# Kernel tuning notes

Hardware: AMD Instinct MI355X
Metric: run time of the kernel (lower is better)

## Reference

```python
import jax, jax.numpy as jnp
import numpy as np

B, IN_DIM, EXP_DIM, E = 16384, 256, 128, 8  # batch, input_dim, expert_dim, expert_num


def setup_inputs() -> dict:
    key = jax.random.key(0)
    ks = jax.random.split(key, 12)
    s_in = 1.0 / np.sqrt(IN_DIM)
    return {
        "x_a": jax.random.normal(ks[0], (B, IN_DIM), jnp.float32),
        "x_b": jax.random.normal(ks[1], (B, IN_DIM), jnp.float32),
        "x_share": jax.random.normal(ks[2], (B, IN_DIM), jnp.float32),
        # expert banks: [E, IN_DIM, EXP_DIM] weights, [E, EXP_DIM] bias
        "Wa": jax.random.uniform(ks[3], (E, IN_DIM, EXP_DIM), jnp.float32, -s_in, s_in),
        "ba": jax.random.uniform(ks[4], (E, EXP_DIM), jnp.float32, -s_in, s_in),
        "Wb": jax.random.uniform(ks[5], (E, IN_DIM, EXP_DIM), jnp.float32, -s_in, s_in),
        "bb": jax.random.uniform(ks[6], (E, EXP_DIM), jnp.float32, -s_in, s_in),
        "Ws": jax.random.uniform(ks[7], (E, IN_DIM, EXP_DIM), jnp.float32, -s_in, s_in),
        "bs": jax.random.uniform(ks[8], (E, EXP_DIM), jnp.float32, -s_in, s_in),
        # gate projections (bias=False): num single-output linears == one [num, IN_DIM] matrix
        "Ga": jax.random.uniform(ks[9], (2 * E, IN_DIM), jnp.float32, -s_in, s_in),
        "Gb": jax.random.uniform(ks[10], (2 * E, IN_DIM), jnp.float32, -s_in, s_in),
        "Gs": jax.random.uniform(ks[11], (3 * E, IN_DIM), jnp.float32, -s_in, s_in),
    }


def _experts(x, W, b):
    # batched dense stack: [B,IN] x [E,IN,D] -> [B,E,D]
    return jnp.einsum("bi,eid->bed", x, W) + b[None, :, :]


def _gate(x, G, experts):
    # logits [B, num]; softmax over experts; weighted sum over expert axis
    w = jax.nn.softmax(x @ G.T, axis=1)
    return jnp.einsum("be,bed->bd", w, experts)


def reference(x_a, x_b, x_share, Wa, ba, Wb, bb, Ws, bs, Ga, Gb, Gs):
    ea = _experts(x_a, Wa, ba)          # [B,E,D]
    eb = _experts(x_b, Wb, bb)          # [B,E,D]
    es = _experts(x_share, Ws, bs)      # [B,E,D]
    out_a = _gate(x_a, Ga, jnp.concatenate([ea, es], axis=1))
    out_b = _gate(x_b, Gb, jnp.concatenate([eb, es], axis=1))
    out_s = _gate(x_share, Gs, jnp.concatenate([ea, eb, es], axis=1))
    return (out_a, out_b, out_s)
```

## Files before the change

kernel.cpp:

```cpp
#include <hip/hip_runtime.h>
#include <stdint.h>

#define BATCH 16384
#define INDIM 256
#define DDIM  128
#define NEXP  8
#define ROWS  64
#define THREADS 512
#define NSTEP 192
#define RINGD 8

typedef __bf16 bfv8  __attribute__((ext_vector_type(8)));
typedef float  f32x4 __attribute__((ext_vector_type(4)));

typedef __attribute__((address_space(1))) const void gas_void;
typedef __attribute__((address_space(3))) void las_void;

__global__ void prep_kernel(const float* __restrict__ Wa, const float* __restrict__ Wb,
                            const float* __restrict__ Ws, const float* __restrict__ Ga,
                            const float* __restrict__ Gb, const float* __restrict__ Gs,
                            __bf16* __restrict__ wp, __bf16* __restrict__ gp) {
    int t = blockIdx.x * 256 + threadIdx.x;
    const int NW = 3 * 8 * 8 * 8 * 64;
    if (t < NW) {
        int lane = t & 63, nt = (t >> 6) & 7, kt = (t >> 9) & 7, e = (t >> 12) & 7, st = t >> 15;
        const float* W = (st == 0) ? Wa : (st == 1) ? Wb : Ws;
        int d  = nt * 16 + (lane & 15);
        int i0 = kt * 32 + (lane >> 4) * 8;
        __bf16* o = wp + (size_t)t * 8;
#pragma unroll
        for (int j = 0; j < 8; j++)
            o[j] = (__bf16)W[(size_t)(e * 256 + i0 + j) * 128 + d];
    } else if (t < NW + 2048) {
        int t2 = t - NW;
        int lane = t2 & 63, nt = (t2 >> 6) & 3, kt = t2 >> 8;
        int g  = nt * 16 + (lane & 15);
        int k0 = kt * 32 + (lane >> 4) * 8;
        __bf16* o = gp + (size_t)t2 * 8;
#pragma unroll
        for (int j = 0; j < 8; j++) {
            int k = k0 + j;
            float v = 0.f;
            if (g < 16)      v = Ga[g * 256 + k];
            else if (g < 32) v = Gb[(g - 16) * 256 + k];
            else if (g < 56) v = Gs[(g - 32) * 256 + k];
            o[j] = (__bf16)v;
        }
    }
}

__device__ __forceinline__ void load_afr(const float* __restrict__ x, int rb,
                                         int l16, int quad, bfv8 afr[2][8]) {
#pragma unroll
    for (int mt = 0; mt < 2; mt++) {
        const float* xr = x + (size_t)(rb + mt * 16 + l16) * INDIM;
#pragma unroll
        for (int kt = 0; kt < 8; kt++) {
            const f32x4* p = (const f32x4*)(xr + kt * 32 + quad * 8);
            f32x4 lo = __builtin_nontemporal_load(p);
            f32x4 hi = __builtin_nontemporal_load(p + 1);
            bfv8 a;
            a[0] = (__bf16)lo[0]; a[1] = (__bf16)lo[1]; a[2] = (__bf16)lo[2]; a[3] = (__bf16)lo[3];
            a[4] = (__bf16)hi[0]; a[5] = (__bf16)hi[1]; a[6] = (__bf16)hi[2]; a[7] = (__bf16)hi[3];
            afr[mt][kt] = a;
        }
    }
}

__device__ __forceinline__ void stage_step(const __bf16* __restrict__ wp,
                                           __bf16* ring, int g, int wv, int lane) {
    const __bf16* src = wp + ((size_t)g << 12) + (wv << 9) + (lane << 3);
    __bf16* dst = ring + ((size_t)(g & (RINGD - 1)) << 12) + (wv << 9);
    __builtin_amdgcn_global_load_lds((gas_void*)src, (las_void*)dst, 16, 0, 0);
}

__launch_bounds__(THREADS, 2)
__global__ void ple_kernel(const float* __restrict__ xa, const float* __restrict__ xb,
                           const float* __restrict__ xs,
                           const float* __restrict__ ba, const float* __restrict__ bb,
                           const float* __restrict__ bs,
                           const __bf16* __restrict__ wp, const __bf16* __restrict__ gp,
                           float* __restrict__ out) {
    __shared__ __bf16 ring[RINGD * 4096];
    __shared__ float lgt[ROWS * 64];
    __shared__ float wT[64 * ROWS];

    const int tid  = threadIdx.x;
    const int wv   = tid >> 6;
    const int lane = tid & 63;
    const int rg   = wv >> 2;
    const int cg   = wv & 3;
    const int quad = lane >> 4;
    const int l16  = lane & 15;
    const int r0   = blockIdx.x * ROWS;
    const int rb   = r0 + rg * 32;

#pragma unroll
    for (int i = 0; i < RINGD - 1; i++) stage_step(wp, ring, i, wv, lane);

    bfv8 afr[2][8];

    {
        const float* x = (cg == 0) ? xa : (cg == 1) ? xb : xs;
        load_afr(x, rb, l16, quad, afr);
        f32x4 acc1[2];
#pragma unroll
        for (int mt = 0; mt < 2; mt++) { f32x4 z = {0.f, 0.f, 0.f, 0.f}; acc1[mt] = z; }
#pragma unroll
        for (int kt = 0; kt < 8; kt++) {
            bfv8 gfr = *(const bfv8*)(gp + ((size_t)(kt * 4 + cg) * 64 + lane) * 8);
#pragma unroll
            for (int mt = 0; mt < 2; mt++)
                acc1[mt] = __builtin_amdgcn_mfma_f32_16x16x32_bf16(afr[mt][kt], gfr, acc1[mt], 0, 0, 0);
        }
#pragma unroll
        for (int mt = 0; mt < 2; mt++)
#pragma unroll
            for (int r = 0; r < 4; r++)
                lgt[(rg * 32 + mt * 16 + quad * 4 + r) * 64 + cg * 16 + l16] = acc1[mt][r];
    }
    __syncthreads();

    if (tid < ROWS) {
        const float* L = lgt + tid * 64;
#pragma unroll
        for (int gi = 0; gi < 3; gi++) {
            const int base = (gi == 0) ? 0 : (gi == 1 ? 16 : 32);
            const int cnt  = (gi == 2) ? 24 : 16;
            float m = -1e30f;
            for (int k = 0; k < cnt; k++) m = fmaxf(m, L[base + k]);
            float s = 0.f;
            for (int k = 0; k < cnt; k++) s += __expf(L[base + k] - m);
            float inv = 1.f / s;
            for (int k = 0; k < cnt; k++) wT[(base + k) * ROWS + tid] = __expf(L[base + k] - m) * inv;
        }
    }
    __syncthreads();

    float o[3][2][2][4];
#pragma unroll
    for (int oi = 0; oi < 3; oi++)
#pragma unroll
        for (int mt = 0; mt < 2; mt++)
#pragma unroll
            for (int ntl = 0; ntl < 2; ntl++)
#pragma unroll
                for (int r = 0; r < 4; r++) o[oi][mt][ntl][r] = 0.f;

#define FOLD(oi, gbase)                                                                 \
    {                                                                                   \
        _Pragma("unroll")                                                               \
        for (int mt = 0; mt < 2; mt++) {                                                \
            f32x4 wv4 = *(const f32x4*)(wT + (gbase + eb) * ROWS + rg * 32 + mt * 16 + quad * 4); \
            _Pragma("unroll")                                                           \
            for (int ntl = 0; ntl < 2; ntl++)                                           \
                _Pragma("unroll")                                                       \
                for (int r = 0; r < 4; r++)                                             \
                    o[oi][mt][ntl][r] += wv4[r] * acc[mt][ntl][r];                      \
        }                                                                               \
    }

#pragma unroll
    for (int st = 0; st < 3; st++) {
        const float* x    = (st == 0) ? xa : (st == 1) ? xb : xs;
        const float* bias = (st == 0) ? ba : (st == 1) ? bb : bs;
        load_afr(x, rb, l16, quad, afr);

#pragma unroll 1
        for (int eb = 0; eb < NEXP; eb++) {
            float b0 = bias[eb * 128 + cg * 32 + l16];
            float b1 = bias[eb * 128 + cg * 32 + 16 + l16];

            f32x4 acc[2][2];
#pragma unroll
            for (int mt = 0; mt < 2; mt++)
#pragma unroll
                for (int ntl = 0; ntl < 2; ntl++) { f32x4 z = {0.f, 0.f, 0.f, 0.f}; acc[mt][ntl] = z; }

#pragma unroll
            for (int kt = 0; kt < 8; kt++) {
                const int g  = st * 64 + eb * 8 + kt;
                const int rem = NSTEP - 1 - g;
                if (rem >= 6)      asm volatile("s_waitcnt vmcnt(6)" ::: "memory");
                else if (rem == 5) asm volatile("s_waitcnt vmcnt(5)" ::: "memory");
                else if (rem == 4) asm volatile("s_waitcnt vmcnt(4)" ::: "memory");
                else if (rem == 3) asm volatile("s_waitcnt vmcnt(3)" ::: "memory");
                else if (rem == 2) asm volatile("s_waitcnt vmcnt(2)" ::: "memory");
                else if (rem == 1) asm volatile("s_waitcnt vmcnt(1)" ::: "memory");
                else               asm volatile("s_waitcnt vmcnt(0)" ::: "memory");
                __builtin_amdgcn_s_barrier();
                asm volatile("" ::: "memory");
                __builtin_amdgcn_sched_barrier(0);
                if (g + RINGD - 1 < NSTEP)
                    stage_step(wp, ring, g + RINGD - 1, wv, lane);

                const __bf16* slab = ring + ((size_t)(g & (RINGD - 1)) << 12) + (cg << 10);
                bfv8 bv0 = *(const bfv8*)(slab + ((size_t)lane << 3));
                bfv8 bv1 = *(const bfv8*)(slab + 512 + ((size_t)lane << 3));
                acc[0][0] = __builtin_amdgcn_mfma_f32_16x16x32_bf16(afr[0][kt], bv0, acc[0][0], 0, 0, 0);
                acc[1][0] = __builtin_amdgcn_mfma_f32_16x16x32_bf16(afr[1][kt], bv0, acc[1][0], 0, 0, 0);
                acc[0][1] = __builtin_amdgcn_mfma_f32_16x16x32_bf16(afr[0][kt], bv1, acc[0][1], 0, 0, 0);
                acc[1][1] = __builtin_amdgcn_mfma_f32_16x16x32_bf16(afr[1][kt], bv1, acc[1][1], 0, 0, 0);
            }

#pragma unroll
            for (int mt = 0; mt < 2; mt++)
#pragma unroll
                for (int r = 0; r < 4; r++) { acc[mt][0][r] += b0; acc[mt][1][r] += b1; }

            if (st == 0)      { FOLD(0, 0);  FOLD(2, 32); }
            else if (st == 1) { FOLD(1, 16); FOLD(2, 40); }
            else              { FOLD(0, 8);  FOLD(1, 24); FOLD(2, 48); }
        }
    }
#undef FOLD

#pragma unroll
    for (int oi = 0; oi < 3; oi++) {
        float* ob = out + (size_t)oi * BATCH * DDIM;
#pragma unroll
        for (int mt = 0; mt < 2; mt++)
#pragma unroll
            for (int r = 0; r < 4; r++) {
                int row = rb + mt * 16 + quad * 4 + r;
#pragma unroll
                for (int ntl = 0; ntl < 2; ntl++)
                    __builtin_nontemporal_store(o[oi][mt][ntl][r],
                        &ob[(size_t)row * DDIM + cg * 32 + ntl * 16 + l16]);
            }
    }
}

extern "C" void kernel_launch(void* const* d_in, const int* in_sizes, int n_in,
                              void* d_out, int out_size, void* d_ws, size_t ws_size,
                              hipStream_t stream) {
    const float* xa = (const float*)d_in[0];
    const float* xb = (const float*)d_in[1];
    const float* xs = (const float*)d_in[2];
    const float* Wa = (const float*)d_in[3];
    const float* ba = (const float*)d_in[4];
    const float* Wb = (const float*)d_in[5];
    const float* bb = (const float*)d_in[6];
    const float* Ws = (const float*)d_in[7];
    const float* bs = (const float*)d_in[8];
    const float* Ga = (const float*)d_in[9];
    const float* Gb = (const float*)d_in[10];
    const float* Gs = (const float*)d_in[11];

    __bf16* wp = (__bf16*)d_ws;
    __bf16* gp = wp + 3 * 8 * 8 * 8 * 64 * 8;

    prep_kernel<<<392, 256, 0, stream>>>(Wa, Wb, Ws, Ga, Gb, Gs, wp, gp);
    ple_kernel<<<BATCH / ROWS, THREADS, 0, stream>>>(xa, xb, xs, ba, bb, bs, wp, gp, (float*)d_out);
}
```

Measured before the change: 181.2 us.

## Replace 8-deep per-k-step LDS ring with double-buffered half-expert staging

New measurement: 186.6 us. +3.0%, slower.

```diff
diff --git a/kernel.cpp b/kernel.cpp
--- a/kernel.cpp
+++ b/kernel.cpp
@@ -7,8 +7,8 @@
 #define NEXP  8
 #define ROWS  64
 #define THREADS 512
-#define NSTEP 192
-#define RINGD 8
+#define NH    48
+#define SLABE 16384
 
 typedef __bf16 bfv8  __attribute__((ext_vector_type(8)));
 typedef float  f32x4 __attribute__((ext_vector_type(4)));
@@ -67,11 +67,14 @@
     }
 }
 
-__device__ __forceinline__ void stage_step(const __bf16* __restrict__ wp,
-                                           __bf16* ring, int g, int wv, int lane) {
-    const __bf16* src = wp + ((size_t)g << 12) + (wv << 9) + (lane << 3);
-    __bf16* dst = ring + ((size_t)(g & (RINGD - 1)) << 12) + (wv << 9);
-    __builtin_amdgcn_global_load_lds((gas_void*)src, (las_void*)dst, 16, 0, 0);
+__device__ __forceinline__ void stage_half(const __bf16* __restrict__ wp,
+                                           __bf16* ring, int h, int wv, int lane) {
+    const __bf16* src = wp + ((size_t)h << 14) + (wv << 11) + (lane << 3);
+    __bf16* dst = ring + ((h & 1) << 14) + (wv << 11);
+#pragma unroll
+    for (int i = 0; i < 4; i++)
+        __builtin_amdgcn_global_load_lds((gas_void*)(src + (i << 9)),
+                                         (las_void*)(dst + (i << 9)), 16, 0, 0);
 }
 
 __launch_bounds__(THREADS, 2)
@@ -81,7 +84,7 @@
                            const float* __restrict__ bs,
                            const __bf16* __restrict__ wp, const __bf16* __restrict__ gp,
                            float* __restrict__ out) {
-    __shared__ __bf16 ring[RINGD * 4096];
+    __shared__ __bf16 ring[2 * SLABE];
     __shared__ float lgt[ROWS * 64];
     __shared__ float wT[64 * ROWS];
 
@@ -95,8 +98,7 @@
     const int r0   = blockIdx.x * ROWS;
     const int rb   = r0 + rg * 32;
 
-#pragma unroll
-    for (int i = 0; i < RINGD - 1; i++) stage_step(wp, ring, i, wv, lane);
+    stage_half(wp, ring, 0, wv, lane);
 
     bfv8 afr[2][8];
 
@@ -151,12 +153,12 @@
     {                                                                                   \
         _Pragma("unroll")                                                               \
         for (int mt = 0; mt < 2; mt++) {                                                \
-            f32x4 wv4 = *(const f32x4*)(wT + (gbase + eb) * ROWS + rg * 32 + mt * 16 + quad * 4); \
+            f32x4 gw4 = *(const f32x4*)(wT + (gbase + eb) * ROWS + rg * 32 + mt * 16 + quad * 4); \
             _Pragma("unroll")                                                           \
             for (int ntl = 0; ntl < 2; ntl++)                                           \
                 _Pragma("unroll")                                                       \
                 for (int r = 0; r < 4; r++)                                             \
-                    o[oi][mt][ntl][r] += wv4[r] * acc[mt][ntl][r];                      \
+                    o[oi][mt][ntl][r] += gw4[r] * acc[mt][ntl][r];                      \
         }                                                                               \
     }
 
@@ -178,29 +180,24 @@
                 for (int ntl = 0; ntl < 2; ntl++) { f32x4 z = {0.f, 0.f, 0.f, 0.f}; acc[mt][ntl] = z; }
 
 #pragma unroll
-            for (int kt = 0; kt < 8; kt++) {
-                const int g  = st * 64 + eb * 8 + kt;
-                const int rem = NSTEP - 1 - g;
-                if (rem >= 6)      asm volatile("s_waitcnt vmcnt(6)" ::: "memory");
-                else if (rem == 5) asm volatile("s_waitcnt vmcnt(5)" ::: "memory");
-                else if (rem == 4) asm volatile("s_waitcnt vmcnt(4)" ::: "memory");
-                else if (rem == 3) asm volatile("s_waitcnt vmcnt(3)" ::: "memory");
-                else if (rem == 2) asm volatile("s_waitcnt vmcnt(2)" ::: "memory");
-                else if (rem == 1) asm volatile("s_waitcnt vmcnt(1)" ::: "memory");
-                else               asm volatile("s_waitcnt vmcnt(0)" ::: "memory");
-                __builtin_amdgcn_s_barrier();
-                asm volatile("" ::: "memory");
-                __builtin_amdgcn_sched_barrier(0);
-                if (g + RINGD - 1 < NSTEP)
-                    stage_step(wp, ring, g + RINGD - 1, wv, lane);
-
-                const __bf16* slab = ring + ((size_t)(g & (RINGD - 1)) << 12) + (cg << 10);
-                bfv8 bv0 = *(const bfv8*)(slab + ((size_t)lane << 3));
-                bfv8 bv1 = *(const bfv8*)(slab + 512 + ((size_t)lane << 3));
-                acc[0][0] = __builtin_amdgcn_mfma_f32_16x16x32_bf16(afr[0][kt], bv0, acc[0][0], 0, 0, 0);
-                acc[1][0] = __builtin_amdgcn_mfma_f32_16x16x32_bf16(afr[1][kt], bv0, acc[1][0], 0, 0, 0);
-                acc[0][1] = __builtin_amdgcn_mfma_f32_16x16x32_bf16(afr[0][kt], bv1, acc[0][1], 0, 0, 0);
-                acc[1][1] = __builtin_amdgcn_mfma_f32_16x16x32_bf16(afr[1][kt], bv1, acc[1][1], 0, 0, 0);
+            for (int half = 0; half < 2; half++) {
+                const int h = st * 16 + eb * 2 + half;
+                __syncthreads();
+                if (h + 1 < NH)
+                    stage_half(wp, ring, h + 1, wv, lane);
+
+                const __bf16* buf = ring + (half << 14);
+#pragma unroll
+                for (int kt4 = 0; kt4 < 4; kt4++) {
+                    const int kt = half * 4 + kt4;
+                    const __bf16* slab = buf + (kt4 << 12) + (cg << 10);
+                    bfv8 bv0 = *(const bfv8*)(slab + ((size_t)lane << 3));
+                    bfv8 bv1 = *(const bfv8*)(slab + 512 + ((size_t)lane << 3));
+                    acc[0][0] = __builtin_amdgcn_mfma_f32_16x16x32_bf16(afr[0][kt], bv0, acc[0][0], 0, 0, 0);
+                    acc[1][0] = __builtin_amdgcn_mfma_f32_16x16x32_bf16(afr[1][kt], bv0, acc[1][0], 0, 0, 0);
+                    acc[0][1] = __builtin_amdgcn_mfma_f32_16x16x32_bf16(afr[0][kt], bv1, acc[0][1], 0, 0, 0);
+                    acc[1][1] = __builtin_amdgcn_mfma_f32_16x16x32_bf16(afr[1][kt], bv1, acc[1][1], 0, 0, 0);
+                }
             }
 
 #pragma unroll
```
